# Kernel tuning notes

Measured on AMD Instinct MI355X. Metric: run time of the kernel, lower is better.

The kernel has to match this reference:

```python
import jax, jax.numpy as jnp
import numpy as np

B, N, C, E = 512, 1000, 50, 128
H, D = 8, 16          # head_num, qkv_dim; H*D == E
CLIP = 10.0           # logit_clipping
NEG = -1e9


def setup_inputs() -> dict:
    key = jax.random.key(0)
    ks = jax.random.split(key, 20)
    f = lambda i, shape, s=1.0: jax.random.normal(ks[i], shape, dtype=jnp.float32) * s
    w = 0.05  # small weight scale so tanh/softmax stay in a sane range
    return dict(
        depot_embedding=f(0, (B, 1, E)),
        cluster_embedding=f(1, (B, C, E)),
        current_embedding=f(2, (B, 1, E)),
        node_embeddings=f(3, (B, N, E)),
        aug_context_embedding=f(4, (B, 1, 4 * E)),
        cluster_guidance_embedding=f(5, (B, 1, E)),
        Wq=f(6, (3 * E, E), w), Wk=f(7, (E, E), w), Wv=f(8, (E, E), w), Wks=f(9, (E, E), w),
        mha_Wq=f(10, (E, H * D), w), mha_Wk=f(11, (E, H * D), w),
        mha_Wv=f(12, (E, H * D), w), mha_Wo=f(13, (H * D, E), w),
        is_new_cluster=jax.random.bernoulli(ks[14], 0.5, (B,)),
        mask=jax.random.bernoulli(ks[15], 0.5, (B, 1, N)),
        cluster_mask=jax.random.bernoulli(ks[16], 0.5, (B, 1, N)),
        visited_cluster_mask=jax.random.bernoulli(ks[17], 0.3, (B, 1, C)),
        cluster_guidance=jax.random.randint(ks[18], (B,), 0, C),
        step=1,
    )


def reference(depot_embedding, cluster_embedding, current_embedding, node_embeddings,
              aug_context_embedding, cluster_guidance_embedding,
              Wq, Wk, Wv, Wks, mha_Wq, mha_Wk, mha_Wv, mha_Wo,
              is_new_cluster, mask, cluster_mask, visited_cluster_mask,
              cluster_guidance, step):
    # step > 0 path: init_* buffers come from the passed-in tensors.
    b, n, e = node_embeddings.shape
    c = cluster_embedding.shape[1]

    def unvisit_embed(m):  # m: [B,1,N] bool, True = visited
        mm = m[:, 0, :, None]                                    # [B,N,1]
        return jnp.where(mm, 0.0, node_embeddings).sum(axis=1, keepdims=True) / n  # [B,1,E]

    # --- new-cluster branch, computed full-batch and selected with where ---
    unvisit_mean = unvisit_embed(mask)                            # [B,1,E]
    context = jnp.concatenate([unvisit_mean, current_embedding, depot_embedding], axis=2)  # [B,1,3E]
    q = context @ Wq                                              # [B,1,E]
    k = cluster_embedding @ Wk                                    # [B,C,E]
    v = cluster_embedding @ Wv                                    # [B,C,E]
    pk = cluster_embedding @ Wks                                  # [B,C,E]

    # if all non-depot clusters visited, unmask cluster 0; else mask it
    all_visited = jnp.all(visited_cluster_mask[:, 0, 1:], axis=1)  # [B]
    vcm = visited_cluster_mask.at[:, 0, 0].set(~all_visited)      # [B,1,C]

    # multi-head glimpse attention
    qh = (q @ mha_Wq).reshape(b, 1, H, D).transpose(0, 2, 1, 3)   # [B,H,1,D]
    kh = (k @ mha_Wk).reshape(b, c, H, D).transpose(0, 2, 1, 3)   # [B,H,C,D]
    vh = (v @ mha_Wv).reshape(b, c, H, D).transpose(0, 2, 1, 3)   # [B,H,C,D]
    scores = jnp.einsum('bhqd,bhkd->bhqk', qh, kh) / jnp.sqrt(jnp.float32(D))
    scores = jnp.where(vcm[:, None, :, :], NEG, scores)           # mask over keys
    attn = jax.nn.softmax(scores, axis=-1)
    glimpse = jnp.einsum('bhqk,bhkd->bhqd', attn, vh)             # [B,H,1,D]
    glimpse = glimpse.transpose(0, 2, 1, 3).reshape(b, 1, H * D) @ mha_Wo  # [B,1,E]

    logit = jnp.einsum('bqe,bce->bqc', glimpse, pk)[:, 0, :] / jnp.sqrt(jnp.float32(e))  # [B,C]
    logit = jnp.tanh(logit) * CLIP
    logit = jnp.where(vcm[:, 0, :], NEG, logit)
    log_p = jax.nn.log_softmax(logit, axis=1)                     # [B,C]

    new_guidance = jnp.argmax(log_p, axis=1)                      # greedy select_mode
    new_guid_embed = jnp.take_along_axis(cluster_embedding, new_guidance[:, None, None], axis=1)  # [B,1,E]

    unvisit_cluster = unvisit_embed(mask | cluster_mask)          # [B,1,E]
    new_aug = jnp.concatenate([unvisit_cluster, current_embedding, new_guid_embed, depot_embedding], axis=2)  # [B,1,4E]

    # --- scatter back: keep old values for rows without a new cluster ---
    is_new = is_new_cluster
    sel3 = is_new[:, None, None]
    aug_out = jnp.where(sel3, new_aug, aug_context_embedding)
    guid_embed_out = jnp.where(sel3, new_guid_embed, cluster_guidance_embedding)
    guid_out = jnp.where(is_new, new_guidance.astype(cluster_guidance.dtype), cluster_guidance)
    clu_prob = jnp.where(is_new[:, None], log_p, 0.0)
    return aug_out, guid_embed_out, guid_out, clu_prob
```

## Files before the change

kernel.cpp:

```cpp
#include <hip/hip_runtime.h>
#include <hip/hip_bf16.h>
#include <math.h>

#define BB 512
#define NN 1000
#define CC 50
#define EE 128
#define HH 8
#define DD 16
#define NEGV (-1000000000.0f)

#define O_AUG 0
#define O_GE  (512*512)
#define O_G   (O_GE + 512*128)
#define O_CP  (O_G + 512)

typedef float vf4 __attribute__((ext_vector_type(4)));

__global__ __launch_bounds__(512) void wprep(
    const float* __restrict__ Wq, const float* __restrict__ Wk,
    const float* __restrict__ Wv, const float* __restrict__ Wks,
    const float* __restrict__ mWq, const float* __restrict__ mWk,
    const float* __restrict__ mWv, const float* __restrict__ Wo,
    float* __restrict__ Wqh, float* __restrict__ Wkh,
    float* __restrict__ Wvh, float* __restrict__ WoKs)
{
    int t   = threadIdx.x;
    int r0  = blockIdx.x * 16;
    int sub = t >> 7;
    int e   = t & 127;
    const float* A; const float* Bm; float* O; int rb; float sc; bool tb;
    if (r0 < 384)      { A = Wq; Bm = mWq; O = Wqh;  rb = r0;       sc = 0.25f; tb = false; }
    else if (r0 < 512) { A = Wk; Bm = mWk; O = Wkh;  rb = r0 - 384; sc = 1.0f;  tb = false; }
    else if (r0 < 640) { A = Wv; Bm = mWv; O = Wvh;  rb = r0 - 512; sc = 1.0f;  tb = false; }
    else               { A = Wo; Bm = Wks; O = WoKs; rb = r0 - 640; sc = 1.0f;  tb = true;  }
    float acc[4] = {0.f, 0.f, 0.f, 0.f};
    if (!tb) {
        for (int i = 0; i < 128; ++i) {
            float bv = Bm[i * 128 + e];
#pragma unroll
            for (int k = 0; k < 4; ++k)
                acc[k] = fmaf(A[(rb + sub + 4 * k) * 128 + i], bv, acc[k]);
        }
    } else {
        for (int i = 0; i < 128; ++i) {
            float bv = Bm[e * 128 + i];
#pragma unroll
            for (int k = 0; k < 4; ++k)
                acc[k] = fmaf(A[(rb + sub + 4 * k) * 128 + i], bv, acc[k]);
        }
    }
#pragma unroll
    for (int k = 0; k < 4; ++k)
        O[(rb + sub + 4 * k) * 128 + e] = acc[k] * sc;
}

__global__ __launch_bounds__(512) void mega(
    const float* __restrict__ node,  const int* __restrict__ mask,
    const int* __restrict__ cmask,
    const float* __restrict__ depot, const float* __restrict__ ce,
    const float* __restrict__ cur,   const float* __restrict__ augc,
    const float* __restrict__ cge,
    const int* __restrict__ isnew_p, const int* __restrict__ vmask,
    const int* __restrict__ guid,
    const float* __restrict__ Wqh,   const float* __restrict__ Wkh,
    const float* __restrict__ Wvh,   const float* __restrict__ WoKs,
    float* __restrict__ out)
{
    int b = blockIdx.x;
    int t = threadIdx.x;

    __shared__ float  sT[128 * 57];
    __shared__ float2 w[1000];
    __shared__ vf4    s1[16][32];
    __shared__ vf4    s2[16][32];
    __shared__ float  sctx[384];
    __shared__ float  suc[128];
    __shared__ float  spq[4][128];
    __shared__ float  sqh[128];
    __shared__ float  sU[8 * 128];
    __shared__ float  sattn[8 * 64];
    __shared__ float  sp[8 * 136];
    __shared__ float  sg[128];
    __shared__ float  sr[128];
    __shared__ float  slog[64];
    __shared__ int    svcm[64];
    __shared__ float  s_m, s_lse;
    __shared__ int    s_arg;

    const int* mb = mask  + b * NN;
    const int* cb = cmask + b * NN;
    for (int n = t; n < NN; n += 512) {
        int m1 = mb[n];
        int m2 = m1 | cb[n];
        w[n] = make_float2(m1 ? 0.f : 1.f, m2 ? 0.f : 1.f);
    }
    const float* ceb = ce + (size_t)b * CC * EE;
    for (int u = t; u < CC * EE; u += 512) {
        int j = u >> 7, i = u & 127;
        sT[i * 57 + j] = ceb[u];
    }
    if (t >= 128 && t < 256) {
        int e = t - 128;
        sctx[128 + e] = cur[b * 128 + e];
        sctx[256 + e] = depot[b * 128 + e];
    }
    if (t >= 256 && t < 320) {
        int j = t - 256;
        svcm[j] = (j < CC) ? vmask[b * CC + j] : 1;
    }
    __syncthreads();

    if (t < 64) {
        int pred = (t >= 1 && t < CC) ? (svcm[t] != 0) : 1;
        int allv = __all(pred);
        if (t == 0) svcm[0] = !allv;
    }

    {
        int v = t & 31, r = t >> 5;
        const vf4* np = (const vf4*)(node + (size_t)b * NN * EE);
        vf4 a1 = {0.f, 0.f, 0.f, 0.f};
        vf4 a2 = {0.f, 0.f, 0.f, 0.f};
        int n = r;
        for (; n + 48 < NN; n += 64) {
            vf4 x0 = __builtin_nontemporal_load(np + (n     ) * 32 + v);
            vf4 x1 = __builtin_nontemporal_load(np + (n + 16) * 32 + v);
            vf4 x2 = __builtin_nontemporal_load(np + (n + 32) * 32 + v);
            vf4 x3 = __builtin_nontemporal_load(np + (n + 48) * 32 + v);
            float2 w0 = w[n], w1 = w[n + 16], w2 = w[n + 32], w3 = w[n + 48];
            a1 += x0 * w0.x; a2 += x0 * w0.y;
            a1 += x1 * w1.x; a2 += x1 * w1.y;
            a1 += x2 * w2.x; a2 += x2 * w2.y;
            a1 += x3 * w3.x; a2 += x3 * w3.y;
        }
        for (; n < NN; n += 16) {
            vf4 x = __builtin_nontemporal_load(np + n * 32 + v);
            float2 ww = w[n];
            a1 += x * ww.x;
            a2 += x * ww.y;
        }
        s1[r][v] = a1;
        s2[r][v] = a2;
    }
    __syncthreads();
    if (t < 128) {
        const float* f1 = (const float*)s1;
        const float* f2 = (const float*)s2;
        float x1 = 0.f, x2 = 0.f;
#pragma unroll
        for (int rr = 0; rr < 16; ++rr) {
            x1 += f1[rr * 128 + t];
            x2 += f2[rr * 128 + t];
        }
        sctx[t] = x1 * (1.0f / (float)NN);
        suc[t]  = x2 * (1.0f / (float)NN);
    }
    __syncthreads();

    {
        int e = t & 127, q4 = t >> 7;
        int i0 = q4 * 96;
        float acc = 0.f;
#pragma unroll 8
        for (int i = 0; i < 96; ++i)
            acc = fmaf(sctx[i0 + i], Wqh[(i0 + i) * 128 + e], acc);
        spq[q4][e] = acc;
    }
    __syncthreads();
    if (t < 128) sqh[t] = (spq[0][t] + spq[1][t]) + (spq[2][t] + spq[3][t]);
    __syncthreads();

    for (int u = t; u < 8 * 128; u += 512) {
        int h = u >> 7, i = u & 127;
        const float* wk = Wkh + i * 128 + h * 16;
        const float* q  = sqh + h * 16;
        float acc = 0.f;
#pragma unroll
        for (int d = 0; d < 16; ++d) acc = fmaf(wk[d], q[d], acc);
        sU[u] = acc;
    }
    __syncthreads();

    if (t < 8 * CC) {
        int h = t / CC, j = t - h * CC;
        float acc = 0.f;
#pragma unroll 8
        for (int i = 0; i < 128; ++i)
            acc = fmaf(sT[i * 57 + j], sU[h * 128 + i], acc);
        sattn[h * 64 + j] = svcm[j] ? NEGV : acc;
    }
    __syncthreads();

    if (t < 256) {
        int h = t >> 5, l = t & 31;
        float s0  = sattn[h * 64 + l];
        float s1v = (l < CC - 32) ? sattn[h * 64 + l + 32] : -INFINITY;
        float m = fmaxf(s0, s1v);
#pragma unroll
        for (int off = 16; off >= 1; off >>= 1)
            m = fmaxf(m, __shfl_xor(m, off, 32));
        float e0 = expf(s0 - m);
        float e1 = (l < CC - 32) ? expf(s1v - m) : 0.f;
        float ssum = e0 + e1;
#pragma unroll
        for (int off = 16; off >= 1; off >>= 1)
            ssum += __shfl_xor(ssum, off, 32);
        float inv = 1.0f / ssum;
        sattn[h * 64 + l] = e0 * inv;
        if (l < CC - 32) sattn[h * 64 + l + 32] = e1 * inv;
    }
    __syncthreads();

    for (int u = t; u < 8 * 128; u += 512) {
        int h = u >> 7, i = u & 127;
        float acc = 0.f;
#pragma unroll
        for (int j = 0; j < CC; ++j)
            acc = fmaf(sattn[h * 64 + j], sT[i * 57 + j], acc);
        sp[h * 136 + i] = acc;
    }
    __syncthreads();

    if (t < 128) {
        int h = t >> 4;
        float acc = 0.f;
#pragma unroll 8
        for (int i = 0; i < 128; ++i)
            acc = fmaf(sp[h * 136 + i], Wvh[i * 128 + t], acc);
        sg[t] = acc;
    }
    __syncthreads();

    if (t < 128) {
        float acc = 0.f;
#pragma unroll 8
        for (int g = 0; g < 128; ++g)
            acc = fmaf(sg[g], WoKs[g * 128 + t], acc);
        sr[t] = acc;
    }
    __syncthreads();

    if (t < 64) {
        if (t < CC) {
            float acc = 0.f;
#pragma unroll 8
            for (int i = 0; i < 128; ++i)
                acc = fmaf(sT[i * 57 + t], sr[i], acc);
            float l = tanhf(acc * 0.08838834764831845f) * 10.0f;
            slog[t] = svcm[t] ? NEGV : l;
        } else {
            slog[t] = NEGV;
        }
    }
    __syncthreads();

    if (t < 64) {
        float val = (t < CC) ? slog[t] : -INFINITY;
        int idx = t;
#pragma unroll
        for (int off = 32; off >= 1; off >>= 1) {
            float ov = __shfl_xor(val, off, 64);
            int   oi = __shfl_xor(idx, off, 64);
            if (ov > val || (ov == val && oi < idx)) { val = ov; idx = oi; }
        }
        float m = val;
        float ex = (t < CC) ? expf(slog[t] - m) : 0.f;
#pragma unroll
        for (int off = 32; off >= 1; off >>= 1)
            ex += __shfl_xor(ex, off, 64);
        if (t == 0) { s_m = m; s_arg = idx; s_lse = logf(ex); }
    }
    __syncthreads();

    bool nw = (isnew_p[b] != 0);
    int  g  = s_arg;
    if (t == 0) {
        out[O_G + b] = nw ? (float)g : (float)guid[b];
    }
    if (t < 128) {
        float nge = sT[t * 57 + g];
        const float* ac = augc + (size_t)b * 512;
        float a0 = nw ? suc[t]             : ac[t];
        float a1 = nw ? sctx[128 + t]      : ac[128 + t];
        float a2 = nw ? nge                : ac[256 + t];
        float a3 = nw ? sctx[256 + t]      : ac[384 + t];
        float* ao = out + O_AUG + (size_t)b * 512;
        ao[t] = a0; ao[128 + t] = a1; ao[256 + t] = a2; ao[384 + t] = a3;
        out[O_GE + b * 128 + t] = nw ? nge : cge[b * 128 + t];
    }
    if (t >= 128 && t < 128 + CC) {
        int j = t - 128;
        out[O_CP + b * CC + j] = nw ? ((slog[j] - s_m) - s_lse) : 0.0f;
    }
}

extern "C" void kernel_launch(void* const* d_in, const int* in_sizes, int n_in,
                              void* d_out, int out_size, void* d_ws, size_t ws_size,
                              hipStream_t stream) {
    const float* depot = (const float*)d_in[0];
    const float* ce    = (const float*)d_in[1];
    const float* cur   = (const float*)d_in[2];
    const float* node  = (const float*)d_in[3];
    const float* augc  = (const float*)d_in[4];
    const float* cge   = (const float*)d_in[5];
    const float* Wq    = (const float*)d_in[6];
    const float* Wk    = (const float*)d_in[7];
    const float* Wv    = (const float*)d_in[8];
    const float* Wks   = (const float*)d_in[9];
    const float* mWq   = (const float*)d_in[10];
    const float* mWk   = (const float*)d_in[11];
    const float* mWv   = (const float*)d_in[12];
    const float* mWo   = (const float*)d_in[13];
    const int*   isnew = (const int*)d_in[14];
    const int*   mask  = (const int*)d_in[15];
    const int*   cmask = (const int*)d_in[16];
    const int*   vmask = (const int*)d_in[17];
    const int*   guid  = (const int*)d_in[18];
    float* out = (float*)d_out;

    float* ws   = (float*)d_ws;
    float* Wqh  = ws;
    float* Wkh  = Wqh  + 384 * 128;
    float* Wvh  = Wkh  + 128 * 128;
    float* WoKs = Wvh  + 128 * 128;

    wprep<<<48, 512, 0, stream>>>(Wq, Wk, Wv, Wks, mWq, mWk, mWv, mWo,
                                  Wqh, Wkh, Wvh, WoKs);
    mega<<<512, 512, 0, stream>>>(node, mask, cmask,
                                  depot, ce, cur, augc, cge,
                                  isnew, vmask, guid,
                                  Wqh, Wkh, Wvh, WoKs, out);
}
```

Baseline: 414.6 us.

## Fuse weight prep into main kernel with atomic flag handoff and split query projection

Removes the separate weight-preparation kernel launch. The first 64 blocks of the main kernel now compute the fused weight products, plus a per-batch projection of current/depot context through Wq and mWq. Each of those blocks signals completion through an atomic counter in workspace, and all blocks spin on that counter before the query stage. This overlaps weight prep with the mask/mean phase and shrinks the per-block query GEMV from 384 to 128 rows. It adds a memset launch, spin-wait synchronisation that assumes the producer blocks are resident, and extra work for the first 64 blocks.

```diff
diff --git a/kernel.cpp b/kernel.cpp
--- a/kernel.cpp
+++ b/kernel.cpp
@@ -15,45 +15,16 @@
 #define O_G   (O_GE + 512*128)
 #define O_CP  (O_G + 512)
 
+#define W_QH0  0
+#define W_KH   (W_QH0 + 128*128)
+#define W_VH   (W_KH  + 128*128)
+#define W_OKS  (W_VH  + 128*128)
+#define W_QCD  (W_OKS + 128*128)
+#define W_FLAG (W_QCD + 512*128)
+
+#define NPROD 64
+
 typedef float vf4 __attribute__((ext_vector_type(4)));
-
-__global__ __launch_bounds__(512) void wprep(
-    const float* __restrict__ Wq, const float* __restrict__ Wk,
-    const float* __restrict__ Wv, const float* __restrict__ Wks,
-    const float* __restrict__ mWq, const float* __restrict__ mWk,
-    const float* __restrict__ mWv, const float* __restrict__ Wo,
-    float* __restrict__ Wqh, float* __restrict__ Wkh,
-    float* __restrict__ Wvh, float* __restrict__ WoKs)
-{
-    int t   = threadIdx.x;
-    int r0  = blockIdx.x * 16;
-    int sub = t >> 7;
-    int e   = t & 127;
-    const float* A; const float* Bm; float* O; int rb; float sc; bool tb;
-    if (r0 < 384)      { A = Wq; Bm = mWq; O = Wqh;  rb = r0;       sc = 0.25f; tb = false; }
-    else if (r0 < 512) { A = Wk; Bm = mWk; O = Wkh;  rb = r0 - 384; sc = 1.0f;  tb = false; }
-    else if (r0 < 640) { A = Wv; Bm = mWv; O = Wvh;  rb = r0 - 512; sc = 1.0f;  tb = false; }
-    else               { A = Wo; Bm = Wks; O = WoKs; rb = r0 - 640; sc = 1.0f;  tb = true;  }
-    float acc[4] = {0.f, 0.f, 0.f, 0.f};
-    if (!tb) {
-        for (int i = 0; i < 128; ++i) {
-            float bv = Bm[i * 128 + e];
-#pragma unroll
-            for (int k = 0; k < 4; ++k)
-                acc[k] = fmaf(A[(rb + sub + 4 * k) * 128 + i], bv, acc[k]);
-        }
-    } else {
-        for (int i = 0; i < 128; ++i) {
-            float bv = Bm[e * 128 + i];
-#pragma unroll
-            for (int k = 0; k < 4; ++k)
-                acc[k] = fmaf(A[(rb + sub + 4 * k) * 128 + i], bv, acc[k]);
-        }
-    }
-#pragma unroll
-    for (int k = 0; k < 4; ++k)
-        O[(rb + sub + 4 * k) * 128 + e] = acc[k] * sc;
-}
 
 __global__ __launch_bounds__(512) void mega(
     const float* __restrict__ node,  const int* __restrict__ mask,
@@ -63,8 +34,11 @@
     const float* __restrict__ cge,
     const int* __restrict__ isnew_p, const int* __restrict__ vmask,
     const int* __restrict__ guid,
-    const float* __restrict__ Wqh,   const float* __restrict__ Wkh,
-    const float* __restrict__ Wvh,   const float* __restrict__ WoKs,
+    const float* __restrict__ Wq,  const float* __restrict__ Wk,
+    const float* __restrict__ Wv,  const float* __restrict__ Wks,
+    const float* __restrict__ mWq, const float* __restrict__ mWk,
+    const float* __restrict__ mWv, const float* __restrict__ Wo,
+    float* __restrict__ ws,
     float* __restrict__ out)
 {
     int b = blockIdx.x;
@@ -88,6 +62,69 @@
     __shared__ float  s_m, s_lse;
     __shared__ int    s_arg;
 
+    int* flag = (int*)(ws + W_FLAG);
+
+    if (b < 32) {
+        int r0  = b * 16;
+        int sub = t >> 7;
+        int e   = t & 127;
+        const float* A; const float* Bm; float* O; int rb; float sc; bool tb;
+        if (r0 < 128)      { A = Wq; Bm = mWq; O = ws + W_QH0; rb = r0;       sc = 0.25f; tb = false; }
+        else if (r0 < 256) { A = Wk; Bm = mWk; O = ws + W_KH;  rb = r0 - 128; sc = 1.0f;  tb = false; }
+        else if (r0 < 384) { A = Wv; Bm = mWv; O = ws + W_VH;  rb = r0 - 256; sc = 1.0f;  tb = false; }
+        else               { A = Wo; Bm = Wks; O = ws + W_OKS; rb = r0 - 384; sc = 1.0f;  tb = true;  }
+        float acc[4] = {0.f, 0.f, 0.f, 0.f};
+        if (!tb) {
+            for (int i = 0; i < 128; ++i) {
+                float bv = Bm[i * 128 + e];
+#pragma unroll
+                for (int k = 0; k < 4; ++k)
+                    acc[k] = fmaf(A[(rb + sub + 4 * k) * 128 + i], bv, acc[k]);
+            }
+        } else {
+            for (int i = 0; i < 128; ++i) {
+                float bv = Bm[e * 128 + i];
+#pragma unroll
+                for (int k = 0; k < 4; ++k)
+                    acc[k] = fmaf(A[(rb + sub + 4 * k) * 128 + i], bv, acc[k]);
+            }
+        }
+#pragma unroll
+        for (int k = 0; k < 4; ++k)
+            O[(rb + sub + 4 * k) * 128 + e] = acc[k] * sc;
+
+        __syncthreads();
+        if (t == 0) {
+            __threadfence();
+            __hip_atomic_fetch_add(flag, 1, __ATOMIC_RELEASE, __HIP_MEMORY_SCOPE_AGENT);
+        }
+    } else if (b < 64) {
+        int bb0 = (b - 32) * 16;
+        int g = t >> 7, e = t & 127;
+        for (int pass = 0; pass < 4; ++pass) {
+            int bb = bb0 + pass * 4 + g;
+            sU[g * 256 + e]       = cur[bb * 128 + e];
+            sU[g * 256 + 128 + e] = depot[bb * 128 + e];
+            __syncthreads();
+            float acc = 0.f;
+#pragma unroll 8
+            for (int i = 0; i < 256; ++i)
+                acc = fmaf(sU[g * 256 + i], Wq[(128 + i) * 128 + e], acc);
+            spq[g][e] = acc;
+            __syncthreads();
+            float acc2 = 0.f;
+#pragma unroll 8
+            for (int d = 0; d < 128; ++d)
+                acc2 = fmaf(spq[g][d], mWq[d * 128 + e], acc2);
+            ws[W_QCD + bb * 128 + e] = acc2 * 0.25f;
+            __syncthreads();
+        }
+        if (t == 0) {
+            __threadfence();
+            __hip_atomic_fetch_add(flag, 1, __ATOMIC_RELEASE, __HIP_MEMORY_SCOPE_AGENT);
+        }
+    }
+
     const int* mb = mask  + b * NN;
     const int* cb = cmask + b * NN;
     for (int n = t; n < NN; n += 512) {
@@ -156,19 +193,31 @@
         sctx[t] = x1 * (1.0f / (float)NN);
         suc[t]  = x2 * (1.0f / (float)NN);
     }
-    __syncthreads();
+
+    if (t == 0) {
+        while (__hip_atomic_load(flag, __ATOMIC_ACQUIRE, __HIP_MEMORY_SCOPE_AGENT) < NPROD) {}
+        __threadfence();
+    }
+    __syncthreads();
+
+    const float* Wqh0 = ws + W_QH0;
+    const float* Wkh  = ws + W_KH;
+    const float* Wvh  = ws + W_VH;
+    const float* WoKs = ws + W_OKS;
 
     {
         int e = t & 127, q4 = t >> 7;
-        int i0 = q4 * 96;
-        float acc = 0.f;
-#pragma unroll 8
-        for (int i = 0; i < 96; ++i)
-            acc = fmaf(sctx[i0 + i], Wqh[(i0 + i) * 128 + e], acc);
+        int i0 = q4 * 32;
+        float acc = 0.f;
+#pragma unroll 8
+        for (int i = 0; i < 32; ++i)
+            acc = fmaf(sctx[i0 + i], Wqh0[(i0 + i) * 128 + e], acc);
         spq[q4][e] = acc;
     }
     __syncthreads();
-    if (t < 128) sqh[t] = (spq[0][t] + spq[1][t]) + (spq[2][t] + spq[3][t]);
+    if (t < 128)
+        sqh[t] = ((spq[0][t] + spq[1][t]) + (spq[2][t] + spq[3][t]))
+               + ws[W_QCD + b * 128 + t];
     __syncthreads();
 
     for (int u = t; u < 8 * 128; u += 512) {
@@ -281,10 +330,10 @@
     if (t < 128) {
         float nge = sT[t * 57 + g];
         const float* ac = augc + (size_t)b * 512;
-        float a0 = nw ? suc[t]             : ac[t];
-        float a1 = nw ? sctx[128 + t]      : ac[128 + t];
-        float a2 = nw ? nge                : ac[256 + t];
-        float a3 = nw ? sctx[256 + t]      : ac[384 + t];
+        float a0 = nw ? suc[t]        : ac[t];
+        float a1 = nw ? sctx[128 + t] : ac[128 + t];
+        float a2 = nw ? nge           : ac[256 + t];
+        float a3 = nw ? sctx[256 + t] : ac[384 + t];
         float* ao = out + O_AUG + (size_t)b * 512;
         ao[t] = a0; ao[128 + t] = a1; ao[256 + t] = a2; ao[384 + t] = a3;
         out[O_GE + b * 128 + t] = nw ? nge : cge[b * 128 + t];
@@ -318,17 +367,13 @@
     const int*   vmask = (const int*)d_in[17];
     const int*   guid  = (const int*)d_in[18];
     float* out = (float*)d_out;
-
-    float* ws   = (float*)d_ws;
-    float* Wqh  = ws;
-    float* Wkh  = Wqh  + 384 * 128;
-    float* Wvh  = Wkh  + 128 * 128;
-    float* WoKs = Wvh  + 128 * 128;
-
-    wprep<<<48, 512, 0, stream>>>(Wq, Wk, Wv, Wks, mWq, mWk, mWv, mWo,
-                                  Wqh, Wkh, Wvh, WoKs);
+    float* ws  = (float*)d_ws;
+
+    hipMemsetAsync((char*)d_ws + W_FLAG * sizeof(float), 0, sizeof(int), stream);
+
     mega<<<512, 512, 0, stream>>>(node, mask, cmask,
                                   depot, ce, cur, augc, cge,
                                   isnew, vmask, guid,
-                                  Wqh, Wkh, Wvh, WoKs, out);
+                                  Wq, Wk, Wv, Wks, mWq, mWk, mWv, mWo,
+                                  ws, out);
 }
```

After: 696.2 us. 67.9% more time.
